# Kernel tuning notes

Hardware: AMD Instinct MI355X
Metric: run time of the kernel (lower is better)

Reference implementation:

```python
import jax, jax.numpy as jnp
import numpy as np

B, H, S, D = 2, 12, 2048, 64

def setup_inputs() -> dict:
    key = jax.random.key(0)
    kq, kk, kv = jax.random.split(key, 3)
    q = jax.random.normal(kq, (B, H, S, D), dtype=jnp.float32)
    k = jax.random.normal(kk, (B, H, S, D), dtype=jnp.float32)
    v = jax.random.normal(kv, (B, H, S, D), dtype=jnp.float32)
    attn_mask = jnp.zeros((1, 1, S, S), dtype=jnp.float32)
    return {"q": q, "k": k, "v": v, "attn_mask": attn_mask}

def reference(q, k, v, attn_mask):
    # scores: [B, H, S, S]
    scale = 1.0 / jnp.sqrt(jnp.asarray(q.shape[-1], q.dtype))
    attn = jnp.einsum('bhqd,bhkd->bhqk', q, k) * scale
    attn = attn + attn_mask  # additive mask, broadcast over batch/heads
    attn = jax.nn.softmax(attn, axis=-1)
    # dropout_ratio == 0.0 -> dropout is identity
    out = jnp.einsum('bhqk,bhkd->bhqd', attn, v)
    return out
```

## Files before the change

### kernel.cpp

```cpp
#include <hip/hip_runtime.h>
#include <hip/hip_bf16.h>
#include <stdint.h>

#define SLEN  2048
#define DHEAD 64
#define LOG2E 1.4426950408889634f
#define QSCALE (0.125f * LOG2E)

typedef short bf16x8 __attribute__((ext_vector_type(8)));
typedef float f32x4  __attribute__((ext_vector_type(4)));
typedef float f32x16 __attribute__((ext_vector_type(16)));
typedef unsigned short u16x8 __attribute__((ext_vector_type(8)));

static __device__ __forceinline__ unsigned short f2bf(float f) {
    union { float f; unsigned int u; } x; x.f = f;
    return (unsigned short)((x.u + 0x7FFFu + ((x.u >> 16) & 1u)) >> 16);
}

static __device__ __forceinline__ unsigned pk2(float lo, float hi) {
    __hip_bfloat162 h = __float22bfloat162_rn(make_float2(lo, hi));
    union { __hip_bfloat162 b; unsigned u; } c; c.b = h; return c.u;
}

static __device__ __forceinline__ void gl_lds16(const void* g, void* l) {
    __builtin_amdgcn_global_load_lds(
        (const __attribute__((address_space(1))) unsigned int*)g,
        (__attribute__((address_space(3))) unsigned int*)l, 16, 0, 0);
}

__global__ __launch_bounds__(256)
void prep(const float* __restrict__ K, const float* __restrict__ V,
          unsigned short* __restrict__ Kb, unsigned short* __restrict__ Vt)
{
    __shared__ unsigned short T[64][72];
    const int tid = threadIdx.x;
    const int st = blockIdx.x, bh = blockIdx.y;
    const size_t base = ((size_t)bh * SLEN + (size_t)st * 64) * DHEAD;

    #pragma unroll
    for (int it = 0; it < 4; ++it) {
        const int idx = it * 1024 + tid * 4;
        const int s = idx >> 6, d = idx & 63;
        float4 k4 = *(const float4*)(K + base + idx);
        float4 v4 = *(const float4*)(V + base + idx);
        ushort4 ko;
        ko.x = f2bf(k4.x); ko.y = f2bf(k4.y);
        ko.z = f2bf(k4.z); ko.w = f2bf(k4.w);
        *(ushort4*)(Kb + base + idx) = ko;
        T[d + 0][s] = f2bf(v4.x);
        T[d + 1][s] = f2bf(v4.y);
        T[d + 2][s] = f2bf(v4.z);
        T[d + 3][s] = f2bf(v4.w);
    }
    __syncthreads();
    const int d = tid >> 2, sc = (tid & 3) * 16;
    unsigned short* orow = Vt + ((size_t)bh * DHEAD + d) * SLEN + (size_t)st * 64 + sc;
    *(u16x8*)(orow)     = *(const u16x8*)&T[d][sc];
    *(u16x8*)(orow + 8) = *(const u16x8*)&T[d][sc + 8];
}

__global__ __launch_bounds__(256, 3)
void sdpa_fwd7(const float* __restrict__ Q,
               const unsigned short* __restrict__ Kb,
               const unsigned short* __restrict__ VtG,
               const float* __restrict__ M, float* __restrict__ O,
               float* __restrict__ Opart, float* __restrict__ ML,
               int nsShift, int BH)
{
    __shared__ unsigned short Kt[3][64][64];
    __shared__ unsigned short Vt[3][64][64];

    const int tid  = threadIdx.x;
    const int wave = tid >> 6, lane = tid & 63;
    const int l31  = lane & 31, hi = lane >> 5;

    const int nwg  = gridDim.x;
    int wg = blockIdx.x;
    if ((nwg & 7) == 0) wg = (wg & 7) * (nwg >> 3) + (wg >> 3);
    const int qt    = wg & 15;
    const int rest  = wg >> 4;
    const int slice = rest & ((1 << nsShift) - 1);
    const int bh    = rest >> nsShift;

    const int kv0 = slice * (SLEN >> nsShift);
    const int NT  = (SLEN >> nsShift) >> 6;
    const int qrow = qt * 128 + wave * 32 + l31;
    const size_t hoff = (size_t)bh * SLEN * DHEAD;

    bf16x8 qf[4];
    {
        const float* qp = Q + hoff + (size_t)qrow * DHEAD + hi * 8;
        #pragma unroll
        for (int ds = 0; ds < 4; ++ds) {
            float4 a = *(const float4*)(qp + ds * 16);
            float4 b = *(const float4*)(qp + ds * 16 + 4);
            union { unsigned u[4]; bf16x8 v; } fq;
            fq.u[0] = pk2(a.x * QSCALE, a.y * QSCALE);
            fq.u[1] = pk2(a.z * QSCALE, a.w * QSCALE);
            fq.u[2] = pk2(b.x * QSCALE, b.y * QSCALE);
            fq.u[3] = pk2(b.z * QSCALE, b.w * QSCALE);
            qf[ds] = fq.v;
        }
    }

    const char* kgb = (const char*)(Kb + hoff) + (size_t)kv0 * 128;
    const char* vgb = (const char*)(VtG + (size_t)bh * DHEAD * SLEN) + (size_t)kv0 * 2;
    unsigned koff[2], voff[2], ldst[2];
    #pragma unroll
    for (int i = 0; i < 2; ++i) {
        const unsigned o = i * 4096 + tid * 16;
        const unsigned row = o >> 7;
        const unsigned slot = ((o >> 4) & 7) ^ (row & 7);
        koff[i] = row * 128 + slot * 16;
        voff[i] = row * 4096 + slot * 16;
        ldst[i] = i * 4096 + wave * 1024;
    }

    f32x16 oacc[2];
    #pragma unroll
    for (int db = 0; db < 2; ++db)
        #pragma unroll
        for (int r = 0; r < 16; ++r) oacc[db][r] = 0.f;
    float m_i = -INFINITY, l_i = 0.f;

    #pragma unroll
    for (int i = 0; i < 2; ++i) {
        gl_lds16(kgb + koff[i], (char*)Kt + ldst[i]);
        gl_lds16(vgb + voff[i], (char*)Vt + ldst[i]);
    }

    int b0 = 0;
    for (int kt = 0; kt < NT; ++kt) {
        const int b1 = (b0 + 1 == 3) ? 0 : b0 + 1;

        if (kt + 1 < NT) {
            #pragma unroll
            for (int i = 0; i < 2; ++i) {
                gl_lds16(kgb + (size_t)(kt + 1) * 8192 + koff[i], (char*)Kt + b1 * 8192 + ldst[i]);
                gl_lds16(vgb + (size_t)(kt + 1) * 128  + voff[i], (char*)Vt + b1 * 8192 + ldst[i]);
            }
            asm volatile("s_waitcnt vmcnt(4)" ::: "memory");
        } else {
            asm volatile("s_waitcnt vmcnt(0)" ::: "memory");
        }
        __builtin_amdgcn_s_barrier();
        __builtin_amdgcn_sched_barrier(0);

        const float* mrow = M + (size_t)qrow * SLEN + kv0 + kt * 64;
        float4 mq[8];
        #pragma unroll
        for (int sb = 0; sb < 2; ++sb)
            #pragma unroll
            for (int g = 0; g < 4; ++g)
                mq[sb * 4 + g] = *(const float4*)(mrow + sb * 32 + g * 8 + hi * 4);

        f32x16 sc[2];
        const char* kl = (const char*)Kt + b0 * 8192;
        __builtin_amdgcn_s_setprio(1);
        #pragma unroll
        for (int sb = 0; sb < 2; ++sb) {
            f32x16 acc;
            #pragma unroll
            for (int r = 0; r < 16; ++r) acc[r] = 0.f;
            const int row = sb * 32 + l31;
            #pragma unroll
            for (int ds = 0; ds < 4; ++ds) {
                const int slot = (ds * 2 + hi) ^ (row & 7);
                bf16x8 kf = *(const bf16x8*)(kl + row * 128 + slot * 16);
                acc = __builtin_amdgcn_mfma_f32_32x32x16_bf16(kf, qf[ds], acc, 0, 0, 0);
            }
            sc[sb] = acc;
        }
        __builtin_amdgcn_s_setprio(0);

        #pragma unroll
        for (int sb = 0; sb < 2; ++sb)
            #pragma unroll
            for (int r = 0; r < 16; ++r)
                sc[sb][r] = fmaf(mq[sb * 4 + (r >> 2)][r & 3], LOG2E, sc[sb][r]);

        float red[16];
        #pragma unroll
        for (int r = 0; r < 16; ++r) red[r] = fmaxf(sc[0][r], sc[1][r]);
        #pragma unroll
        for (int r = 0; r < 8; ++r) red[r] = fmaxf(red[r], red[r + 8]);
        #pragma unroll
        for (int r = 0; r < 4; ++r) red[r] = fmaxf(red[r], red[r + 4]);
        red[0] = fmaxf(fmaxf(red[0], red[2]), fmaxf(red[1], red[3]));
        const float mtile = fmaxf(red[0], __shfl_xor(red[0], 32));

        if (!__all(mtile - m_i <= 11.0f)) {
            const float mnew = fmaxf(m_i, mtile);
            const float alpha = __builtin_amdgcn_exp2f(m_i - mnew);
            l_i *= alpha;
            #pragma unroll
            for (int db = 0; db < 2; ++db)
                #pragma unroll
                for (int r = 0; r < 16; ++r) oacc[db][r] *= alpha;
            m_i = mnew;
        }

        #pragma unroll
        for (int sb = 0; sb < 2; ++sb)
            #pragma unroll
            for (int r = 0; r < 16; ++r)
                sc[sb][r] = __builtin_amdgcn_exp2f(sc[sb][r] - m_i);

        unsigned wa[8], wb[8];
        #pragma unroll
        for (int sb = 0; sb < 2; ++sb)
            #pragma unroll
            for (int g = 0; g < 4; ++g) {
                wa[sb * 4 + g] = pk2(sc[sb][4 * g + 0], sc[sb][4 * g + 1]);
                wb[sb * 4 + g] = pk2(sc[sb][4 * g + 2], sc[sb][4 * g + 3]);
            }
        bf16x8 pf[4];
        #pragma unroll
        for (int ks = 0; ks < 4; ++ks) {
            const int base = (ks >> 1) * 4 + (ks & 1) * 2;
            const unsigned a = wa[base], b = wa[base + 1];
            const unsigned c = wb[base], d = wb[base + 1];
            const unsigned z0 = hi ? a : b;
            const unsigned z1 = hi ? c : d;
            const unsigned w0 = (unsigned)__shfl_xor((int)z0, 32);
            const unsigned w1 = (unsigned)__shfl_xor((int)z1, 32);
            union { unsigned u[4]; bf16x8 v; } f;
            f.u[0] = hi ? w0 : a;
            f.u[1] = hi ? w1 : c;
            f.u[2] = hi ? b : w0;
            f.u[3] = hi ? d : w1;
            pf[ks] = f.v;
        }

        const char* vl = (const char*)Vt + b0 * 8192;
        __builtin_amdgcn_s_setprio(1);
        #pragma unroll
        for (int db = 0; db < 2; ++db) {
            const int row = db * 32 + l31;
            #pragma unroll
            for (int ks = 0; ks < 4; ++ks) {
                const int slot = (ks * 2 + hi) ^ (row & 7);
                bf16x8 vf = *(const bf16x8*)(vl + row * 128 + slot * 16);
                oacc[db] = __builtin_amdgcn_mfma_f32_32x32x16_bf16(vf, pf[ks], oacc[db], 0, 0, 0);
            }
        }
        __builtin_amdgcn_s_setprio(0);

        float sr[16];
        #pragma unroll
        for (int r = 0; r < 16; ++r) sr[r] = sc[0][r] + sc[1][r];
        #pragma unroll
        for (int r = 0; r < 8; ++r) sr[r] += sr[r + 8];
        #pragma unroll
        for (int r = 0; r < 4; ++r) sr[r] += sr[r + 4];
        sr[0] = (sr[0] + sr[2]) + (sr[1] + sr[3]);
        l_i += sr[0] + __shfl_xor(sr[0], 32);

        b0 = b1;
    }

    if (nsShift == 0) {
        const float inv = 1.0f / l_i;
        float* op = O + hoff + (size_t)qrow * DHEAD;
        #pragma unroll
        for (int db = 0; db < 2; ++db)
            #pragma unroll
            for (int g = 0; g < 4; ++g) {
                float4 o4;
                o4.x = oacc[db][4 * g + 0] * inv;
                o4.y = oacc[db][4 * g + 1] * inv;
                o4.z = oacc[db][4 * g + 2] * inv;
                o4.w = oacc[db][4 * g + 3] * inv;
                *(float4*)(op + db * 32 + g * 8 + hi * 4) = o4;
            }
    } else {
        const size_t pidx = ((size_t)slice * BH + bh) * SLEN + qrow;
        float* op = Opart + pidx * DHEAD;
        #pragma unroll
        for (int db = 0; db < 2; ++db)
            #pragma unroll
            for (int g = 0; g < 4; ++g) {
                float4 o4;
                o4.x = oacc[db][4 * g + 0];
                o4.y = oacc[db][4 * g + 1];
                o4.z = oacc[db][4 * g + 2];
                o4.w = oacc[db][4 * g + 3];
                *(float4*)(op + db * 32 + g * 8 + hi * 4) = o4;
            }
        if (hi == 0) {
            ML[pidx * 2]     = m_i;
            ML[pidx * 2 + 1] = l_i;
        }
    }
}

__global__ __launch_bounds__(256)
void merge_partials(const float* __restrict__ Opart, const float* __restrict__ ML,
                    float* __restrict__ O, int NS, int BHS)
{
    const int gid = blockIdx.x * 256 + threadIdx.x;
    const int row = gid >> 4;
    const int c = (gid & 15) << 2;
    if (row >= BHS) return;

    float m = -INFINITY;
    for (int s = 0; s < NS; ++s)
        m = fmaxf(m, ML[((size_t)s * BHS + row) * 2]);

    float lsum = 0.f;
    float4 acc = make_float4(0.f, 0.f, 0.f, 0.f);
    for (int s = 0; s < NS; ++s) {
        const size_t pr = (size_t)s * BHS + row;
        const float w = __builtin_amdgcn_exp2f(ML[pr * 2] - m);
        lsum += w * ML[pr * 2 + 1];
        float4 v = *(const float4*)(Opart + pr * DHEAD + c);
        acc.x += w * v.x; acc.y += w * v.y;
        acc.z += w * v.z; acc.w += w * v.w;
    }
    const float inv = 1.0f / lsum;
    float4 o4;
    o4.x = acc.x * inv; o4.y = acc.y * inv;
    o4.z = acc.z * inv; o4.w = acc.w * inv;
    *(float4*)(O + (size_t)row * DHEAD + c) = o4;
}

__global__ __launch_bounds__(256)
void sdpa_fwd(const float* __restrict__ Q, const float* __restrict__ K,
              const float* __restrict__ V, const float* __restrict__ M,
              float* __restrict__ O)
{
    __shared__ unsigned short Klds[64][72];
    __shared__ unsigned short Vtl[64][72];
    __shared__ unsigned short Plds[4][16][72];

    const int tid  = threadIdx.x;
    const int wave = tid >> 6, lane = tid & 63;
    const int lg   = lane >> 4, ln = lane & 15;
    const int qtile = blockIdx.x, bh = blockIdx.y;
    const int qbase = qtile * 64 + wave * 16;
    const size_t hoff = (size_t)bh * SLEN * DHEAD;

    bf16x8 qf[2];
    {
        const float* qp = Q + hoff + (size_t)(qbase + ln) * DHEAD;
        #pragma unroll
        for (int ks = 0; ks < 2; ++ks) {
            float4 a = *(const float4*)(qp + ks * 32 + lg * 8);
            float4 b = *(const float4*)(qp + ks * 32 + lg * 8 + 4);
            qf[ks][0] = (short)f2bf(a.x * 0.125f); qf[ks][1] = (short)f2bf(a.y * 0.125f);
            qf[ks][2] = (short)f2bf(a.z * 0.125f); qf[ks][3] = (short)f2bf(a.w * 0.125f);
            qf[ks][4] = (short)f2bf(b.x * 0.125f); qf[ks][5] = (short)f2bf(b.y * 0.125f);
            qf[ks][6] = (short)f2bf(b.z * 0.125f); qf[ks][7] = (short)f2bf(b.w * 0.125f);
        }
    }

    f32x4 oacc[4];
    #pragma unroll
    for (int dn = 0; dn < 4; ++dn) oacc[dn] = (f32x4){0.f, 0.f, 0.f, 0.f};
    float m_i[4] = {-INFINITY, -INFINITY, -INFINITY, -INFINITY};
    float l_i[4] = {0.f, 0.f, 0.f, 0.f};

    for (int kt = 0; kt < SLEN / 64; ++kt) {
        const int kbase = kt * 64;
        __syncthreads();
        {
            const float* kp = K + hoff + (size_t)kbase * DHEAD;
            const float* vp = V + hoff + (size_t)kbase * DHEAD;
            #pragma unroll
            for (int it = 0; it < 4; ++it) {
                int flat = it * 1024 + tid * 4;
                int r = flat >> 6, c = flat & 63;
                float4 kv4 = *(const float4*)(kp + flat);
                float4 vv4 = *(const float4*)(vp + flat);
                ushort4 kb;
                kb.x = f2bf(kv4.x); kb.y = f2bf(kv4.y);
                kb.z = f2bf(kv4.z); kb.w = f2bf(kv4.w);
                *(ushort4*)&Klds[r][c] = kb;
                Vtl[c + 0][r] = f2bf(vv4.x); Vtl[c + 1][r] = f2bf(vv4.y);
                Vtl[c + 2][r] = f2bf(vv4.z); Vtl[c + 3][r] = f2bf(vv4.w);
            }
        }
        __syncthreads();

        f32x4 sc[4];
        #pragma unroll
        for (int nt = 0; nt < 4; ++nt) {
            f32x4 acc = (f32x4){0.f, 0.f, 0.f, 0.f};
            #pragma unroll
            for (int ks = 0; ks < 2; ++ks) {
                bf16x8 kf = *(const bf16x8*)&Klds[nt * 16 + ln][ks * 32 + lg * 8];
                acc = __builtin_amdgcn_mfma_f32_16x16x32_bf16(qf[ks], kf, acc, 0, 0, 0);
            }
            sc[nt] = acc;
        }
        #pragma unroll
        for (int i = 0; i < 4; ++i) {
            const float* mrow = M + (size_t)(qbase + 4 * lg + i) * SLEN + kbase;
            #pragma unroll
            for (int nt = 0; nt < 4; ++nt) sc[nt][i] += mrow[nt * 16 + ln];
        }
        float mnew[4], alpha[4];
        #pragma unroll
        for (int i = 0; i < 4; ++i) {
            float tm = fmaxf(fmaxf(sc[0][i], sc[1][i]), fmaxf(sc[2][i], sc[3][i]));
            tm = fmaxf(tm, __shfl_xor(tm, 1));
            tm = fmaxf(tm, __shfl_xor(tm, 2));
            tm = fmaxf(tm, __shfl_xor(tm, 4));
            tm = fmaxf(tm, __shfl_xor(tm, 8));
            mnew[i] = fmaxf(m_i[i], tm);
            alpha[i] = __expf(m_i[i] - mnew[i]);
            m_i[i] = mnew[i];
        }
        #pragma unroll
        for (int nt = 0; nt < 4; ++nt)
            #pragma unroll
            for (int i = 0; i < 4; ++i) {
                float p = __expf(sc[nt][i] - mnew[i]);
                sc[nt][i] = p;
                Plds[wave][4 * lg + i][nt * 16 + ln] = f2bf(p);
            }
        #pragma unroll
        for (int i = 0; i < 4; ++i) {
            float ts = (sc[0][i] + sc[1][i]) + (sc[2][i] + sc[3][i]);
            ts += __shfl_xor(ts, 1);
            ts += __shfl_xor(ts, 2);
            ts += __shfl_xor(ts, 4);
            ts += __shfl_xor(ts, 8);
            l_i[i] = l_i[i] * alpha[i] + ts;
            #pragma unroll
            for (int dn = 0; dn < 4; ++dn) oacc[dn][i] *= alpha[i];
        }
        #pragma unroll
        for (int ks = 0; ks < 2; ++ks) {
            bf16x8 pa = *(const bf16x8*)&Plds[wave][ln][ks * 32 + lg * 8];
            #pragma unroll
            for (int dn = 0; dn < 4; ++dn) {
                bf16x8 vb = *(const bf16x8*)&Vtl[dn * 16 + ln][ks * 32 + lg * 8];
                oacc[dn] = __builtin_amdgcn_mfma_f32_16x16x32_bf16(pa, vb, oacc[dn], 0, 0, 0);
            }
        }
    }
    #pragma unroll
    for (int i = 0; i < 4; ++i) {
        float inv = 1.0f / l_i[i];
        float* op = O + hoff + (size_t)(qbase + 4 * lg + i) * DHEAD;
        #pragma unroll
        for (int dn = 0; dn < 4; ++dn) op[dn * 16 + ln] = oacc[dn][i] * inv;
    }
}

extern "C" void kernel_launch(void* const* d_in, const int* in_sizes, int n_in,
                              void* d_out, int out_size, void* d_ws, size_t ws_size,
                              hipStream_t stream) {
    const float* q = (const float*)d_in[0];
    const float* k = (const float*)d_in[1];
    const float* v = (const float*)d_in[2];
    const float* m = (const float*)d_in[3];
    float* o = (float*)d_out;

    const int bh = in_sizes[0] / (SLEN * DHEAD);
    const size_t H = (size_t)bh * SLEN * DHEAD;
    const size_t BHS = (size_t)bh * SLEN;
    const size_t baseB = 2 * H * sizeof(unsigned short);

    if (ws_size < baseB) {
        sdpa_fwd<<<dim3(SLEN / 64, bh), 256, 0, stream>>>(q, k, v, m, o);
        return;
    }

    const size_t perS = H * sizeof(float) + BHS * 2 * sizeof(float);
    int nsShift = (ws_size >= baseB + 2 * perS) ? 1 : 0;
    const int NS = 1 << nsShift;

    unsigned short* kb = (unsigned short*)d_ws;
    unsigned short* vt = kb + H;
    float* opart = (float*)((char*)d_ws + baseB);
    float* ml    = opart + (size_t)NS * H;

    prep<<<dim3(SLEN / 64, bh), 256, 0, stream>>>(k, v, kb, vt);
    sdpa_fwd7<<<16 * bh * NS, 256, 0, stream>>>(q, kb, vt, m, o, opart, ml, nsShift, bh);
    if (NS > 1) {
        const int mb = (int)((BHS * 16 + 255) / 256);
        merge_partials<<<mb, 256, 0, stream>>>(opart, ml, o, NS, (int)BHS);
    }
}
```

Baseline: 80.71 us.

## Software-pipeline QK^T of next tile with softmax/PV of current tile

Restructures the attention main loop so the QK^T MFMAs for tile t+1 are issued before the softmax and PV of tile t, letting matrix work overlap the exp/reduction work. The global-to-LDS prefetch now runs two tiles ahead across the triple buffer, with the wait and barrier moved accordingly. The loop is unrolled by two to ping-pong score registers. This costs extra VGPRs for a second score set, which may pressure occupancy under launch_bounds(256,3). The loop assumes an even tile count.

```diff
diff --git a/kernel.cpp b/kernel.cpp
--- a/kernel.cpp
+++ b/kernel.cpp
@@ -60,7 +60,7 @@
 }
 
 __global__ __launch_bounds__(256, 3)
-void sdpa_fwd7(const float* __restrict__ Q,
+void sdpa_fwd8(const float* __restrict__ Q,
                const unsigned short* __restrict__ Kb,
                const unsigned short* __restrict__ VtG,
                const float* __restrict__ M, float* __restrict__ O,
@@ -123,39 +123,17 @@
         for (int r = 0; r < 16; ++r) oacc[db][r] = 0.f;
     float m_i = -INFINITY, l_i = 0.f;
 
-    #pragma unroll
-    for (int i = 0; i < 2; ++i) {
-        gl_lds16(kgb + koff[i], (char*)Kt + ldst[i]);
-        gl_lds16(vgb + voff[i], (char*)Vt + ldst[i]);
-    }
-
-    int b0 = 0;
-    for (int kt = 0; kt < NT; ++kt) {
-        const int b1 = (b0 + 1 == 3) ? 0 : b0 + 1;
-
-        if (kt + 1 < NT) {
-            #pragma unroll
-            for (int i = 0; i < 2; ++i) {
-                gl_lds16(kgb + (size_t)(kt + 1) * 8192 + koff[i], (char*)Kt + b1 * 8192 + ldst[i]);
-                gl_lds16(vgb + (size_t)(kt + 1) * 128  + voff[i], (char*)Vt + b1 * 8192 + ldst[i]);
-            }
-            asm volatile("s_waitcnt vmcnt(4)" ::: "memory");
-        } else {
-            asm volatile("s_waitcnt vmcnt(0)" ::: "memory");
-        }
-        __builtin_amdgcn_s_barrier();
-        __builtin_amdgcn_sched_barrier(0);
-
-        const float* mrow = M + (size_t)qrow * SLEN + kv0 + kt * 64;
-        float4 mq[8];
-        #pragma unroll
-        for (int sb = 0; sb < 2; ++sb)
-            #pragma unroll
-            for (int g = 0; g < 4; ++g)
-                mq[sb * 4 + g] = *(const float4*)(mrow + sb * 32 + g * 8 + hi * 4);
-
-        f32x16 sc[2];
-        const char* kl = (const char*)Kt + b0 * 8192;
+    auto STAGE = [&](int tt) {
+        const unsigned bo = (unsigned)(tt % 3) * 8192;
+        #pragma unroll
+        for (int i = 0; i < 2; ++i) {
+            gl_lds16(kgb + (size_t)tt * 8192 + koff[i], (char*)Kt + bo + ldst[i]);
+            gl_lds16(vgb + (size_t)tt * 128  + voff[i], (char*)Vt + bo + ldst[i]);
+        }
+    };
+
+    auto QK = [&](int tt, f32x16& s0, f32x16& s1) {
+        const char* kl = (const char*)Kt + (tt % 3) * 8192;
         __builtin_amdgcn_s_setprio(1);
         #pragma unroll
         for (int sb = 0; sb < 2; ++sb) {
@@ -169,19 +147,38 @@
                 bf16x8 kf = *(const bf16x8*)(kl + row * 128 + slot * 16);
                 acc = __builtin_amdgcn_mfma_f32_32x32x16_bf16(kf, qf[ds], acc, 0, 0, 0);
             }
-            sc[sb] = acc;
+            if (sb == 0) s0 = acc; else s1 = acc;
         }
         __builtin_amdgcn_s_setprio(0);
-
+    };
+
+    auto BODY = [&](int t, f32x16& c0, f32x16& c1, f32x16& n0, f32x16& n1) {
+        asm volatile("" ::: "memory");
+        const float* mrow = M + (size_t)qrow * SLEN + kv0 + t * 64;
+        float4 mq[8];
         #pragma unroll
         for (int sb = 0; sb < 2; ++sb)
             #pragma unroll
-            for (int r = 0; r < 16; ++r)
-                sc[sb][r] = fmaf(mq[sb * 4 + (r >> 2)][r & 3], LOG2E, sc[sb][r]);
+            for (int g = 0; g < 4; ++g)
+                mq[sb * 4 + g] = *(const float4*)(mrow + sb * 32 + g * 8 + hi * 4);
+
+        asm volatile("s_waitcnt vmcnt(8)" ::: "memory");
+        __builtin_amdgcn_s_barrier();
+        __builtin_amdgcn_sched_barrier(0);
+
+        if (t + 2 < NT) STAGE(t + 2);
+
+        #pragma unroll
+        for (int r = 0; r < 16; ++r) {
+            c0[r] = fmaf(mq[(r >> 2)][r & 3], LOG2E, c0[r]);
+            c1[r] = fmaf(mq[4 + (r >> 2)][r & 3], LOG2E, c1[r]);
+        }
+
+        if (t + 1 < NT) QK(t + 1, n0, n1);
 
         float red[16];
         #pragma unroll
-        for (int r = 0; r < 16; ++r) red[r] = fmaxf(sc[0][r], sc[1][r]);
+        for (int r = 0; r < 16; ++r) red[r] = fmaxf(c0[r], c1[r]);
         #pragma unroll
         for (int r = 0; r < 8; ++r) red[r] = fmaxf(red[r], red[r + 8]);
         #pragma unroll
@@ -201,19 +198,29 @@
         }
 
         #pragma unroll
-        for (int sb = 0; sb < 2; ++sb)
-            #pragma unroll
-            for (int r = 0; r < 16; ++r)
-                sc[sb][r] = __builtin_amdgcn_exp2f(sc[sb][r] - m_i);
+        for (int r = 0; r < 16; ++r) {
+            c0[r] = __builtin_amdgcn_exp2f(c0[r] - m_i);
+            c1[r] = __builtin_amdgcn_exp2f(c1[r] - m_i);
+        }
+
+        float sr[16];
+        #pragma unroll
+        for (int r = 0; r < 16; ++r) sr[r] = c0[r] + c1[r];
+        #pragma unroll
+        for (int r = 0; r < 8; ++r) sr[r] += sr[r + 8];
+        #pragma unroll
+        for (int r = 0; r < 4; ++r) sr[r] += sr[r + 4];
+        sr[0] = (sr[0] + sr[2]) + (sr[1] + sr[3]);
+        l_i += sr[0] + __shfl_xor(sr[0], 32);
 
         unsigned wa[8], wb[8];
         #pragma unroll
-        for (int sb = 0; sb < 2; ++sb)
-            #pragma unroll
-            for (int g = 0; g < 4; ++g) {
-                wa[sb * 4 + g] = pk2(sc[sb][4 * g + 0], sc[sb][4 * g + 1]);
-                wb[sb * 4 + g] = pk2(sc[sb][4 * g + 2], sc[sb][4 * g + 3]);
-            }
+        for (int g = 0; g < 4; ++g) {
+            wa[g]     = pk2(c0[4 * g + 0], c0[4 * g + 1]);
+            wb[g]     = pk2(c0[4 * g + 2], c0[4 * g + 3]);
+            wa[4 + g] = pk2(c1[4 * g + 0], c1[4 * g + 1]);
+            wb[4 + g] = pk2(c1[4 * g + 2], c1[4 * g + 3]);
+        }
         bf16x8 pf[4];
         #pragma unroll
         for (int ks = 0; ks < 4; ++ks) {
@@ -232,7 +239,7 @@
             pf[ks] = f.v;
         }
 
-        const char* vl = (const char*)Vt + b0 * 8192;
+        const char* vl = (const char*)Vt + (t % 3) * 8192;
         __builtin_amdgcn_s_setprio(1);
         #pragma unroll
         for (int db = 0; db < 2; ++db) {
@@ -245,18 +252,18 @@
             }
         }
         __builtin_amdgcn_s_setprio(0);
-
-        float sr[16];
-        #pragma unroll
-        for (int r = 0; r < 16; ++r) sr[r] = sc[0][r] + sc[1][r];
-        #pragma unroll
-        for (int r = 0; r < 8; ++r) sr[r] += sr[r + 8];
-        #pragma unroll
-        for (int r = 0; r < 4; ++r) sr[r] += sr[r + 4];
-        sr[0] = (sr[0] + sr[2]) + (sr[1] + sr[3]);
-        l_i += sr[0] + __shfl_xor(sr[0], 32);
-
-        b0 = b1;
+    };
+
+    STAGE(0); STAGE(1);
+    asm volatile("s_waitcnt vmcnt(4)" ::: "memory");
+    __builtin_amdgcn_s_barrier();
+    __builtin_amdgcn_sched_barrier(0);
+    f32x16 sA0, sA1, sB0, sB1;
+    QK(0, sA0, sA1);
+
+    for (int t = 0; t < NT; t += 2) {
+        BODY(t,     sA0, sA1, sB0, sB1);
+        BODY(t + 1, sB0, sB1, sA0, sA1);
     }
 
     if (nsShift == 0) {
@@ -478,7 +485,7 @@
     float* ml    = opart + (size_t)NS * H;
 
     prep<<<dim3(SLEN / 64, bh), 256, 0, stream>>>(k, v, kb, vt);
-    sdpa_fwd7<<<16 * bh * NS, 256, 0, stream>>>(q, kb, vt, m, o, opart, ml, nsShift, bh);
+    sdpa_fwd8<<<16 * bh * NS, 256, 0, stream>>>(q, kb, vt, m, o, opart, ml, nsShift, bh);
     if (NS > 1) {
         const int mb = (int)((BHS * 16 + 255) / 256);
         merge_partials<<<mb, 256, 0, stream>>>(opart, ml, o, NS, (int)BHS);
```

New measurement: 131.9 us. 63.4% more time.

## Use permlane32 swaps, fold mask into MFMA init, reswizzle LDS, hoist mask loads

Applied to the files above, without the earlier changes.

Replaces the ds_bpermute-based cross-half shuffles for the P fragment, the row max and the row sum with the gfx950 permlane32_swap instruction. The additive mask is now used to initialise the QK^T MFMA accumulator instead of being added afterwards, and the mask global loads are issued before the staging wait so their latency overlaps the barrier. The LDS XOR swizzle gains a second term (row>>3) to change the bank-conflict pattern, and the row-sum reduction moves before the PV MFMAs. Moving the mask loads earlier keeps more registers live across the barrier, and the vmcnt(4) wait must still account for the mask loads correctly.

```diff
diff --git a/kernel.cpp b/kernel.cpp
--- a/kernel.cpp
+++ b/kernel.cpp
@@ -11,6 +11,7 @@
 typedef float f32x4  __attribute__((ext_vector_type(4)));
 typedef float f32x16 __attribute__((ext_vector_type(16)));
 typedef unsigned short u16x8 __attribute__((ext_vector_type(8)));
+typedef unsigned u32x2 __attribute__((ext_vector_type(2)));
 
 static __device__ __forceinline__ unsigned short f2bf(float f) {
     union { float f; unsigned int u; } x; x.f = f;
@@ -21,6 +22,12 @@
     __hip_bfloat162 h = __float22bfloat162_rn(make_float2(lo, hi));
     union { __hip_bfloat162 b; unsigned u; } c; c.b = h; return c.u;
 }
+
+static __device__ __forceinline__ u32x2 pl32(unsigned a, unsigned b) {
+    return __builtin_amdgcn_permlane32_swap(a, b, false, false);
+}
+static __device__ __forceinline__ float    asf(unsigned u) { union { unsigned u; float f; } c; c.u = u; return c.f; }
+static __device__ __forceinline__ unsigned asu(float f)    { union { float f; unsigned u; } c; c.f = f; return c.u; }
 
 static __device__ __forceinline__ void gl_lds16(const void* g, void* l) {
     __builtin_amdgcn_global_load_lds(
@@ -60,7 +67,7 @@
 }
 
 __global__ __launch_bounds__(256, 3)
-void sdpa_fwd7(const float* __restrict__ Q,
+void sdpa_fwd9(const float* __restrict__ Q,
                const unsigned short* __restrict__ Kb,
                const unsigned short* __restrict__ VtG,
                const float* __restrict__ M, float* __restrict__ O,
@@ -110,7 +117,7 @@
     for (int i = 0; i < 2; ++i) {
         const unsigned o = i * 4096 + tid * 16;
         const unsigned row = o >> 7;
-        const unsigned slot = ((o >> 4) & 7) ^ (row & 7);
+        const unsigned slot = ((o >> 4) & 7) ^ (row & 7) ^ ((row >> 3) & 7);
         koff[i] = row * 128 + slot * 16;
         voff[i] = row * 4096 + slot * 16;
         ldst[i] = i * 4096 + wave * 1024;
@@ -123,22 +130,31 @@
         for (int r = 0; r < 16; ++r) oacc[db][r] = 0.f;
     float m_i = -INFINITY, l_i = 0.f;
 
-    #pragma unroll
-    for (int i = 0; i < 2; ++i) {
-        gl_lds16(kgb + koff[i], (char*)Kt + ldst[i]);
-        gl_lds16(vgb + voff[i], (char*)Vt + ldst[i]);
-    }
-
-    int b0 = 0;
+    auto STAGE = [&](int tt) {
+        const unsigned bo = (unsigned)(tt % 3) * 8192;
+        #pragma unroll
+        for (int i = 0; i < 2; ++i) {
+            gl_lds16(kgb + (size_t)tt * 8192 + koff[i], (char*)Kt + bo + ldst[i]);
+            gl_lds16(vgb + (size_t)tt * 128  + voff[i], (char*)Vt + bo + ldst[i]);
+        }
+    };
+
+    STAGE(0);
+
     for (int kt = 0; kt < NT; ++kt) {
-        const int b1 = (b0 + 1 == 3) ? 0 : b0 + 1;
+        const int b0 = kt % 3;
+
+        const float* mrow = M + (size_t)qrow * SLEN + kv0 + kt * 64;
+        float4 mq[8];
+        #pragma unroll
+        for (int sb = 0; sb < 2; ++sb)
+            #pragma unroll
+            for (int g = 0; g < 4; ++g)
+                mq[sb * 4 + g] = *(const float4*)(mrow + sb * 32 + g * 8 + hi * 4);
+        asm volatile("" ::: "memory");
 
         if (kt + 1 < NT) {
-            #pragma unroll
-            for (int i = 0; i < 2; ++i) {
-                gl_lds16(kgb + (size_t)(kt + 1) * 8192 + koff[i], (char*)Kt + b1 * 8192 + ldst[i]);
-                gl_lds16(vgb + (size_t)(kt + 1) * 128  + voff[i], (char*)Vt + b1 * 8192 + ldst[i]);
-            }
+            STAGE(kt + 1);
             asm volatile("s_waitcnt vmcnt(4)" ::: "memory");
         } else {
             asm volatile("s_waitcnt vmcnt(0)" ::: "memory");
@@ -146,14 +162,6 @@
         __builtin_amdgcn_s_barrier();
         __builtin_amdgcn_sched_barrier(0);
 
-        const float* mrow = M + (size_t)qrow * SLEN + kv0 + kt * 64;
-        float4 mq[8];
-        #pragma unroll
-        for (int sb = 0; sb < 2; ++sb)
-            #pragma unroll
-            for (int g = 0; g < 4; ++g)
-                mq[sb * 4 + g] = *(const float4*)(mrow + sb * 32 + g * 8 + hi * 4);
-
         f32x16 sc[2];
         const char* kl = (const char*)Kt + b0 * 8192;
         __builtin_amdgcn_s_setprio(1);
@@ -161,11 +169,13 @@
         for (int sb = 0; sb < 2; ++sb) {
             f32x16 acc;
             #pragma unroll
-            for (int r = 0; r < 16; ++r) acc[r] = 0.f;
+            for (int r = 0; r < 16; ++r)
+                acc[r] = mq[sb * 4 + (r >> 2)][r & 3] * LOG2E;
             const int row = sb * 32 + l31;
+            const int rx = (row & 7) ^ ((row >> 3) & 7);
             #pragma unroll
             for (int ds = 0; ds < 4; ++ds) {
-                const int slot = (ds * 2 + hi) ^ (row & 7);
+                const int slot = (ds * 2 + hi) ^ rx;
                 bf16x8 kf = *(const bf16x8*)(kl + row * 128 + slot * 16);
                 acc = __builtin_amdgcn_mfma_f32_32x32x16_bf16(kf, qf[ds], acc, 0, 0, 0);
             }
@@ -173,12 +183,6 @@
         }
         __builtin_amdgcn_s_setprio(0);
 
-        #pragma unroll
-        for (int sb = 0; sb < 2; ++sb)
-            #pragma unroll
-            for (int r = 0; r < 16; ++r)
-                sc[sb][r] = fmaf(mq[sb * 4 + (r >> 2)][r & 3], LOG2E, sc[sb][r]);
-
         float red[16];
         #pragma unroll
         for (int r = 0; r < 16; ++r) red[r] = fmaxf(sc[0][r], sc[1][r]);
@@ -187,7 +191,8 @@
         #pragma unroll
         for (int r = 0; r < 4; ++r) red[r] = fmaxf(red[r], red[r + 4]);
         red[0] = fmaxf(fmaxf(red[0], red[2]), fmaxf(red[1], red[3]));
-        const float mtile = fmaxf(red[0], __shfl_xor(red[0], 32));
+        u32x2 pm = pl32(asu(red[0]), asu(red[0]));
+        const float mtile = fmaxf(asf(pm.x), asf(pm.y));
 
         if (!__all(mtile - m_i <= 11.0f)) {
             const float mnew = fmaxf(m_i, mtile);
@@ -206,6 +211,17 @@
             for (int r = 0; r < 16; ++r)
                 sc[sb][r] = __builtin_amdgcn_exp2f(sc[sb][r] - m_i);
 
+        float sr[16];
+        #pragma unroll
+        for (int r = 0; r < 16; ++r) sr[r] = sc[0][r] + sc[1][r];
+        #pragma unroll
+        for (int r = 0; r < 8; ++r) sr[r] += sr[r + 8];
+        #pragma unroll
+        for (int r = 0; r < 4; ++r) sr[r] += sr[r + 4];
+        sr[0] = (sr[0] + sr[2]) + (sr[1] + sr[3]);
+        u32x2 ps = pl32(asu(sr[0]), asu(sr[0]));
+        l_i += asf(ps.x) + asf(ps.y);
+
         unsigned wa[8], wb[8];
         #pragma unroll
         for (int sb = 0; sb < 2; ++sb)
@@ -217,18 +233,13 @@
         bf16x8 pf[4];
         #pragma unroll
         for (int ks = 0; ks < 4; ++ks) {
-            const int base = (ks >> 1) * 4 + (ks & 1) * 2;
-            const unsigned a = wa[base], b = wa[base + 1];
-            const unsigned c = wb[base], d = wb[base + 1];
-            const unsigned z0 = hi ? a : b;
-            const unsigned z1 = hi ? c : d;
-            const unsigned w0 = (unsigned)__shfl_xor((int)z0, 32);
-            const unsigned w1 = (unsigned)__shfl_xor((int)z1, 32);
+            u32x2 pa = pl32(wa[2 * ks], wa[2 * ks + 1]);
+            u32x2 pb = pl32(wb[2 * ks], wb[2 * ks + 1]);
             union { unsigned u[4]; bf16x8 v; } f;
-            f.u[0] = hi ? w0 : a;
-            f.u[1] = hi ? w1 : c;
-            f.u[2] = hi ? b : w0;
-            f.u[3] = hi ? d : w1;
+            f.u[0] = pa.x;
+            f.u[1] = pb.x;
+            f.u[2] = pa.y;
+            f.u[3] = pb.y;
             pf[ks] = f.v;
         }
 
@@ -237,26 +248,15 @@
         #pragma unroll
         for (int db = 0; db < 2; ++db) {
             const int row = db * 32 + l31;
+            const int rx = (row & 7) ^ ((row >> 3) & 7);
             #pragma unroll
             for (int ks = 0; ks < 4; ++ks) {
-                const int slot = (ks * 2 + hi) ^ (row & 7);
+                const int slot = (ks * 2 + hi) ^ rx;
                 bf16x8 vf = *(const bf16x8*)(vl + row * 128 + slot * 16);
                 oacc[db] = __builtin_amdgcn_mfma_f32_32x32x16_bf16(vf, pf[ks], oacc[db], 0, 0, 0);
             }
         }
         __builtin_amdgcn_s_setprio(0);
-
-        float sr[16];
-        #pragma unroll
-        for (int r = 0; r < 16; ++r) sr[r] = sc[0][r] + sc[1][r];
-        #pragma unroll
-        for (int r = 0; r < 8; ++r) sr[r] += sr[r + 8];
-        #pragma unroll
-        for (int r = 0; r < 4; ++r) sr[r] += sr[r + 4];
-        sr[0] = (sr[0] + sr[2]) + (sr[1] + sr[3]);
-        l_i += sr[0] + __shfl_xor(sr[0], 32);
-
-        b0 = b1;
     }
 
     if (nsShift == 0) {
@@ -478,7 +478,7 @@
     float* ml    = opart + (size_t)NS * H;
 
     prep<<<dim3(SLEN / 64, bh), 256, 0, stream>>>(k, v, kb, vt);
-    sdpa_fwd7<<<16 * bh * NS, 256, 0, stream>>>(q, kb, vt, m, o, opart, ml, nsShift, bh);
+    sdpa_fwd9<<<16 * bh * NS, 256, 0, stream>>>(q, kb, vt, m, o, opart, ml, nsShift, bh);
     if (NS > 1) {
         const int mb = (int)((BHS * 16 + 255) / 256);
         merge_partials<<<mb, 256, 0, stream>>>(opart, ml, o, NS, (int)BHS);
```

Result: slower. 88.81 us (+10.0%).
